# Performance work log

Hardware: AMD Instinct MI355X
Metric: run time of the kernel (lower is better)

## Reference

```python
import jax, jax.numpy as jnp
import numpy as np

B, N, M, K = 1024, 20000, 10000, 8
CHK_W, OBS_W = 8, 200          # fixed support size per check / observable row
EPS = 1e-6
BETA = 0.5


def setup_inputs() -> dict:
    rng = np.random.default_rng(0)
    # packed CSR-style support sets (fixed row weight -> dense index tables)
    chk_cols = jnp.asarray(rng.integers(0, N, size=(M, CHK_W)), dtype=jnp.int32)
    obs_cols = jnp.asarray(rng.integers(0, N, size=(K, OBS_W)), dtype=jnp.int32)
    key = jax.random.key(0)
    k1, k2, k3 = jax.random.split(key, 3)
    llrs = jax.random.normal(k1, (B, N), dtype=jnp.float32) * 2.0
    syndromes = jax.random.bernoulli(k2, 0.5, (B, M)).astype(jnp.float32)
    observables = jax.random.bernoulli(k3, 0.5, (B, K)).astype(jnp.float32)
    return {"llrs": llrs, "syndromes": syndromes, "observables": observables,
            "chk_cols": chk_cols, "obs_cols": obs_cols}


def _pred_llr(tanh_half, cols):
    # tanh_half: (B, N); cols: (R, W) -> gathered (B, R, W)
    g = tanh_half[:, cols]
    prod = jnp.prod(g, axis=-1)                       # BP check-node tanh product, (B, R)
    prod = jnp.clip(prod, -1.0 + EPS, 1.0 - EPS)
    return 2.0 * jnp.arctanh(prod)


def _bce_with_logits(z, y):
    # BCEWithLogitsLoss(z, y) = softplus(z) - z*y (numerically stable)
    return jax.nn.softplus(z) - z * y


def reference(llrs, syndromes, observables, chk_cols, obs_cols):
    t = jnp.tanh(llrs * 0.5)                          # (B, N)
    syn_pred_llr = _pred_llr(t, chk_cols)             # (B, M)
    obs_pred_llr = _pred_llr(t, obs_cols)             # (B, K)
    loss1 = _bce_with_logits(-syn_pred_llr, syndromes).sum(axis=1)
    loss2 = _bce_with_logits(-obs_pred_llr, observables).sum(axis=1)
    loss = BETA * loss1 + (1.0 - BETA) * loss2
    return loss.mean()
```

## Files before the change

### kernel.cpp

```cpp
#include <hip/hip_runtime.h>

#define B_ 1024
#define N_ 20000
#define M_ 10000
#define K_ 8
#define OBS_W_ 200
#define TPB 1024

constexpr float EPS_   = 1e-6f;
constexpr float LN2_   = 0.69314718055994530942f;
constexpr float LOG2E_ = 1.4426950408889634f;

typedef _Float16 f16x2 __attribute__((ext_vector_type(2)));
typedef _Float16 f16x8 __attribute__((ext_vector_type(8)));

__device__ __forceinline__ float tanh_half_fast(float x) {
    float e = __builtin_amdgcn_exp2f(x * LOG2E_);
    return 1.0f - 2.0f * __builtin_amdgcn_rcpf(e + 1.0f);
}

template <bool ATOMIC>
__global__ __launch_bounds__(TPB) void decode_loss_main2(
    const float* __restrict__ llrs,
    const float* __restrict__ syndromes,
    const float* __restrict__ observables,
    const int*   __restrict__ chk_cols,
    const int*   __restrict__ obs_cols,
    float* __restrict__ part)
{
    extern __shared__ char smem_raw[];
    f16x2* t2 = reinterpret_cast<f16x2*>(smem_raw);
    __shared__ float red0[TPB / 64], red1[TPB / 64];

    const int b0  = 2 * blockIdx.x;
    const int b1  = b0 + 1;
    const int tid = threadIdx.x;

    const float4* r0 = reinterpret_cast<const float4*>(llrs + (size_t)b0 * N_);
    const float4* r1 = reinterpret_cast<const float4*>(llrs + (size_t)b1 * N_);
    for (int i = tid; i < N_ / 4; i += TPB) {
        float4 a = r0[i];
        float4 c = r1[i];
        f16x8 v;
        v[0] = (_Float16)tanh_half_fast(a.x); v[1] = (_Float16)tanh_half_fast(c.x);
        v[2] = (_Float16)tanh_half_fast(a.y); v[3] = (_Float16)tanh_half_fast(c.y);
        v[4] = (_Float16)tanh_half_fast(a.z); v[5] = (_Float16)tanh_half_fast(c.z);
        v[6] = (_Float16)tanh_half_fast(a.w); v[7] = (_Float16)tanh_half_fast(c.w);
        *reinterpret_cast<f16x8*>(&t2[4 * i]) = v;
    }
    __syncthreads();

    float acc0 = 0.0f, acc1 = 0.0f;
    int   cnt  = 0;
    const float* syn0 = syndromes + (size_t)b0 * M_;
    const float* syn1 = syndromes + (size_t)b1 * M_;
    const int4*  cc   = reinterpret_cast<const int4*>(chk_cols);
    for (int m = tid; m < M_; m += TPB) {
        int4 c0 = cc[2 * m];
        int4 c1 = cc[2 * m + 1];
        f16x2 g0 = t2[c0.x], g1 = t2[c0.y], g2 = t2[c0.z], g3 = t2[c0.w];
        f16x2 g4 = t2[c1.x], g5 = t2[c1.y], g6 = t2[c1.z], g7 = t2[c1.w];
        f16x2 p  = ((g0 * g1) * (g2 * g3)) * ((g4 * g5) * (g6 * g7));
        float pa = (float)p[0];
        float pb = (float)p[1];
        pa = fminf(fmaxf(pa, -1.0f + EPS_), 1.0f - EPS_);
        pb = fminf(fmaxf(pb, -1.0f + EPS_), 1.0f - EPS_);
        float w0 = fmaf(1.0f - 2.0f * syn0[m], pa, 1.0f);
        float w1 = fmaf(1.0f - 2.0f * syn1[m], pb, 1.0f);
        acc0 += __builtin_amdgcn_logf(w0);
        acc1 += __builtin_amdgcn_logf(w1);
        ++cnt;
    }
    float sum0 = 0.5f * LN2_ * ((float)cnt - acc0);
    float sum1 = 0.5f * LN2_ * ((float)cnt - acc1);

    if (tid < 128) {
        const int row = tid >> 6;
        const int k   = (tid >> 3) & 7;
        const int seg = tid & 7;
        const int* oc = obs_cols + k * OBS_W_ + seg * 25;
        float pr = 1.0f;
        #pragma unroll 5
        for (int w = 0; w < 25; ++w) {
            f16x2 g = t2[oc[w]];
            pr *= (float)g[row];
        }
        #pragma unroll
        for (int off = 1; off < 8; off <<= 1) pr *= __shfl_xor(pr, off, 64);
        if (seg == 0) {
            const int bb = row == 0 ? b0 : b1;
            float p = fminf(fmaxf(pr, -1.0f + EPS_), 1.0f - EPS_);
            float sgn = 1.0f - 2.0f * observables[(size_t)bb * K_ + k];
            float w2  = fmaf(sgn, p, 1.0f);
            float v   = 0.5f * LN2_ * (1.0f - __builtin_amdgcn_logf(w2));
            if (row == 0) sum0 += v; else sum1 += v;
        }
    }

    for (int off = 32; off > 0; off >>= 1) {
        sum0 += __shfl_down(sum0, off, 64);
        sum1 += __shfl_down(sum1, off, 64);
    }
    const int lane = tid & 63, wv = tid >> 6;
    if (lane == 0) { red0[wv] = sum0; red1[wv] = sum1; }
    __syncthreads();
    if (tid == 0) {
        float tot = 0.0f;
        #pragma unroll
        for (int i = 0; i < TPB / 64; ++i) tot += red0[i] + red1[i];
        if (ATOMIC) {
            atomicAdd(part, tot * (1.0f / (float)B_));
        } else {
            part[blockIdx.x] = tot;
        }
    }
}

__global__ __launch_bounds__(256) void decode_loss_reduce(
    const float* __restrict__ part, float* __restrict__ out, int n)
{
    __shared__ float red[4];
    const int tid = threadIdx.x;
    float s = 0.0f;
    for (int i = tid; i < n; i += 256) s += part[i];
    for (int off = 32; off > 0; off >>= 1) s += __shfl_down(s, off, 64);
    const int lane = tid & 63, wv = tid >> 6;
    if (lane == 0) red[wv] = s;
    __syncthreads();
    if (tid == 0) out[0] = (red[0] + red[1] + red[2] + red[3]) * (1.0f / (float)B_);
}

extern "C" void kernel_launch(void* const* d_in, const int* in_sizes, int n_in,
                              void* d_out, int out_size, void* d_ws, size_t ws_size,
                              hipStream_t stream) {
    const float* llrs        = (const float*)d_in[0];
    const float* syndromes   = (const float*)d_in[1];
    const float* observables = (const float*)d_in[2];
    const int*   chk_cols    = (const int*)d_in[3];
    const int*   obs_cols    = (const int*)d_in[4];
    float*       out         = (float*)d_out;

    const size_t lds_bytes = (size_t)N_ * sizeof(f16x2);

    static_assert(sizeof(f16x2) == 4, "");
    {
        auto kf = decode_loss_main2<false>;
        auto kt = decode_loss_main2<true>;
        (void)hipFuncSetAttribute((const void*)kf,
            hipFuncAttributeMaxDynamicSharedMemorySize, (int)lds_bytes);
        (void)hipFuncSetAttribute((const void*)kt,
            hipFuncAttributeMaxDynamicSharedMemorySize, (int)lds_bytes);
    }

    const int nblk = B_ / 2;
    if (ws_size >= (size_t)nblk * sizeof(float)) {
        float* part = (float*)d_ws;
        decode_loss_main2<false><<<nblk, TPB, lds_bytes, stream>>>(
            llrs, syndromes, observables, chk_cols, obs_cols, part);
        decode_loss_reduce<<<1, 256, 0, stream>>>(part, out, nblk);
    } else {
        hipMemsetAsync(out, 0, sizeof(float), stream);
        decode_loss_main2<true><<<nblk, TPB, lds_bytes, stream>>>(
            llrs, syndromes, observables, chk_cols, obs_cols, out);
    }
}
```

Measured before the change: 29.74 us.

## Process four batch rows per block with interleaved f16x4 tanh table in LDS

Adds a kernel variant in which each block handles four batch rows instead of two. The tanh values are stored interleaved as f16x4 in 160KB of LDS, so each gather of a check column serves four samples and chk_cols is read once per four rows. The aim is to amortize index loads and LDS gather instructions over more rows. In exchange it halves the block count to 256, which may be fewer than the number of CUs, and uses more LDS per block. It falls back to the two-row kernel if the LDS attribute cannot be set.

```diff
diff --git a/kernel.cpp b/kernel.cpp
--- a/kernel.cpp
+++ b/kernel.cpp
@@ -12,11 +12,107 @@
 constexpr float LOG2E_ = 1.4426950408889634f;
 
 typedef _Float16 f16x2 __attribute__((ext_vector_type(2)));
+typedef _Float16 f16x4 __attribute__((ext_vector_type(4)));
 typedef _Float16 f16x8 __attribute__((ext_vector_type(8)));
 
 __device__ __forceinline__ float tanh_half_fast(float x) {
     float e = __builtin_amdgcn_exp2f(x * LOG2E_);
     return 1.0f - 2.0f * __builtin_amdgcn_rcpf(e + 1.0f);
+}
+
+__device__ __forceinline__ float bce_term(float p, float y) {
+    p = fminf(fmaxf(p, -1.0f + EPS_), 1.0f - EPS_);
+    float w = fmaf(1.0f - 2.0f * y, p, 1.0f);
+    return __builtin_amdgcn_logf(w);
+}
+
+template <bool ATOMIC>
+__global__ __launch_bounds__(TPB) void decode_loss_main4(
+    const float* __restrict__ llrs,
+    const float* __restrict__ syndromes,
+    const float* __restrict__ observables,
+    const int*   __restrict__ chk_cols,
+    const int*   __restrict__ obs_cols,
+    float* __restrict__ part)
+{
+    extern __shared__ char smem_raw[];
+    f16x4* t4 = reinterpret_cast<f16x4*>(smem_raw);
+    __shared__ float red[TPB / 64];
+
+    const int b0  = 4 * blockIdx.x;
+    const int tid = threadIdx.x;
+
+    const float4* r0 = reinterpret_cast<const float4*>(llrs + (size_t)(b0 + 0) * N_);
+    const float4* r1 = reinterpret_cast<const float4*>(llrs + (size_t)(b0 + 1) * N_);
+    const float4* r2 = reinterpret_cast<const float4*>(llrs + (size_t)(b0 + 2) * N_);
+    const float4* r3 = reinterpret_cast<const float4*>(llrs + (size_t)(b0 + 3) * N_);
+    for (int i = tid; i < N_ / 4; i += TPB) {
+        float4 a = r0[i], b = r1[i], c = r2[i], d = r3[i];
+        f16x8 w01, w23;
+        w01[0] = (_Float16)tanh_half_fast(a.x); w01[1] = (_Float16)tanh_half_fast(b.x);
+        w01[2] = (_Float16)tanh_half_fast(c.x); w01[3] = (_Float16)tanh_half_fast(d.x);
+        w01[4] = (_Float16)tanh_half_fast(a.y); w01[5] = (_Float16)tanh_half_fast(b.y);
+        w01[6] = (_Float16)tanh_half_fast(c.y); w01[7] = (_Float16)tanh_half_fast(d.y);
+        w23[0] = (_Float16)tanh_half_fast(a.z); w23[1] = (_Float16)tanh_half_fast(b.z);
+        w23[2] = (_Float16)tanh_half_fast(c.z); w23[3] = (_Float16)tanh_half_fast(d.z);
+        w23[4] = (_Float16)tanh_half_fast(a.w); w23[5] = (_Float16)tanh_half_fast(b.w);
+        w23[6] = (_Float16)tanh_half_fast(c.w); w23[7] = (_Float16)tanh_half_fast(d.w);
+        *reinterpret_cast<f16x8*>(&t4[4 * i + 0]) = w01;
+        *reinterpret_cast<f16x8*>(&t4[4 * i + 2]) = w23;
+    }
+    __syncthreads();
+
+    float acc = 0.0f;
+    int   cnt = 0;
+    const float* syn0 = syndromes + (size_t)(b0 + 0) * M_;
+    const float* syn1 = syndromes + (size_t)(b0 + 1) * M_;
+    const float* syn2 = syndromes + (size_t)(b0 + 2) * M_;
+    const float* syn3 = syndromes + (size_t)(b0 + 3) * M_;
+    const int4*  cc   = reinterpret_cast<const int4*>(chk_cols);
+    for (int m = tid; m < M_; m += TPB) {
+        int4 c0 = cc[2 * m];
+        int4 c1 = cc[2 * m + 1];
+        f16x4 g0 = t4[c0.x], g1 = t4[c0.y], g2 = t4[c0.z], g3 = t4[c0.w];
+        f16x4 g4 = t4[c1.x], g5 = t4[c1.y], g6 = t4[c1.z], g7 = t4[c1.w];
+        f16x4 p  = ((g0 * g1) * (g2 * g3)) * ((g4 * g5) * (g6 * g7));
+        acc += bce_term((float)p[0], syn0[m]);
+        acc += bce_term((float)p[1], syn1[m]);
+        acc += bce_term((float)p[2], syn2[m]);
+        acc += bce_term((float)p[3], syn3[m]);
+        ++cnt;
+    }
+    float sum = 0.5f * LN2_ * (4.0f * (float)cnt - acc);
+
+    if (tid < 256) {
+        const int row = tid >> 6;
+        const int k   = (tid >> 3) & 7;
+        const int seg = tid & 7;
+        const int* oc = obs_cols + k * OBS_W_ + seg * 25;
+        float pr = 1.0f;
+        #pragma unroll 5
+        for (int w = 0; w < 25; ++w) {
+            f16x4 g = t4[oc[w]];
+            pr *= (float)g[row];
+        }
+        #pragma unroll
+        for (int off = 1; off < 8; off <<= 1) pr *= __shfl_xor(pr, off, 64);
+        if (seg == 0) {
+            float y = observables[(size_t)(b0 + row) * K_ + k];
+            sum += 0.5f * LN2_ * (1.0f - bce_term(pr, y));
+        }
+    }
+
+    for (int off = 32; off > 0; off >>= 1) sum += __shfl_down(sum, off, 64);
+    const int lane = tid & 63, wv = tid >> 6;
+    if (lane == 0) red[wv] = sum;
+    __syncthreads();
+    if (tid == 0) {
+        float tot = 0.0f;
+        #pragma unroll
+        for (int i = 0; i < TPB / 64; ++i) tot += red[i];
+        if (ATOMIC) atomicAdd(part, tot * (1.0f / (float)B_));
+        else        part[blockIdx.x] = tot;
+    }
 }
 
 template <bool ATOMIC>
@@ -30,17 +126,15 @@
 {
     extern __shared__ char smem_raw[];
     f16x2* t2 = reinterpret_cast<f16x2*>(smem_raw);
-    __shared__ float red0[TPB / 64], red1[TPB / 64];
+    __shared__ float red[TPB / 64];
 
     const int b0  = 2 * blockIdx.x;
-    const int b1  = b0 + 1;
     const int tid = threadIdx.x;
 
     const float4* r0 = reinterpret_cast<const float4*>(llrs + (size_t)b0 * N_);
-    const float4* r1 = reinterpret_cast<const float4*>(llrs + (size_t)b1 * N_);
+    const float4* r1 = reinterpret_cast<const float4*>(llrs + (size_t)(b0 + 1) * N_);
     for (int i = tid; i < N_ / 4; i += TPB) {
-        float4 a = r0[i];
-        float4 c = r1[i];
+        float4 a = r0[i], c = r1[i];
         f16x8 v;
         v[0] = (_Float16)tanh_half_fast(a.x); v[1] = (_Float16)tanh_half_fast(c.x);
         v[2] = (_Float16)tanh_half_fast(a.y); v[3] = (_Float16)tanh_half_fast(c.y);
@@ -50,10 +144,10 @@
     }
     __syncthreads();
 
-    float acc0 = 0.0f, acc1 = 0.0f;
-    int   cnt  = 0;
+    float acc = 0.0f;
+    int   cnt = 0;
     const float* syn0 = syndromes + (size_t)b0 * M_;
-    const float* syn1 = syndromes + (size_t)b1 * M_;
+    const float* syn1 = syndromes + (size_t)(b0 + 1) * M_;
     const int4*  cc   = reinterpret_cast<const int4*>(chk_cols);
     for (int m = tid; m < M_; m += TPB) {
         int4 c0 = cc[2 * m];
@@ -61,18 +155,11 @@
         f16x2 g0 = t2[c0.x], g1 = t2[c0.y], g2 = t2[c0.z], g3 = t2[c0.w];
         f16x2 g4 = t2[c1.x], g5 = t2[c1.y], g6 = t2[c1.z], g7 = t2[c1.w];
         f16x2 p  = ((g0 * g1) * (g2 * g3)) * ((g4 * g5) * (g6 * g7));
-        float pa = (float)p[0];
-        float pb = (float)p[1];
-        pa = fminf(fmaxf(pa, -1.0f + EPS_), 1.0f - EPS_);
-        pb = fminf(fmaxf(pb, -1.0f + EPS_), 1.0f - EPS_);
-        float w0 = fmaf(1.0f - 2.0f * syn0[m], pa, 1.0f);
-        float w1 = fmaf(1.0f - 2.0f * syn1[m], pb, 1.0f);
-        acc0 += __builtin_amdgcn_logf(w0);
-        acc1 += __builtin_amdgcn_logf(w1);
+        acc += bce_term((float)p[0], syn0[m]);
+        acc += bce_term((float)p[1], syn1[m]);
         ++cnt;
     }
-    float sum0 = 0.5f * LN2_ * ((float)cnt - acc0);
-    float sum1 = 0.5f * LN2_ * ((float)cnt - acc1);
+    float sum = 0.5f * LN2_ * (2.0f * (float)cnt - acc);
 
     if (tid < 128) {
         const int row = tid >> 6;
@@ -81,38 +168,25 @@
         const int* oc = obs_cols + k * OBS_W_ + seg * 25;
         float pr = 1.0f;
         #pragma unroll 5
-        for (int w = 0; w < 25; ++w) {
-            f16x2 g = t2[oc[w]];
-            pr *= (float)g[row];
-        }
+        for (int w = 0; w < 25; ++w) { f16x2 g = t2[oc[w]]; pr *= (float)g[row]; }
         #pragma unroll
         for (int off = 1; off < 8; off <<= 1) pr *= __shfl_xor(pr, off, 64);
         if (seg == 0) {
-            const int bb = row == 0 ? b0 : b1;
-            float p = fminf(fmaxf(pr, -1.0f + EPS_), 1.0f - EPS_);
-            float sgn = 1.0f - 2.0f * observables[(size_t)bb * K_ + k];
-            float w2  = fmaf(sgn, p, 1.0f);
-            float v   = 0.5f * LN2_ * (1.0f - __builtin_amdgcn_logf(w2));
-            if (row == 0) sum0 += v; else sum1 += v;
+            float y = observables[(size_t)(b0 + row) * K_ + k];
+            sum += 0.5f * LN2_ * (1.0f - bce_term(pr, y));
         }
     }
 
-    for (int off = 32; off > 0; off >>= 1) {
-        sum0 += __shfl_down(sum0, off, 64);
-        sum1 += __shfl_down(sum1, off, 64);
-    }
+    for (int off = 32; off > 0; off >>= 1) sum += __shfl_down(sum, off, 64);
     const int lane = tid & 63, wv = tid >> 6;
-    if (lane == 0) { red0[wv] = sum0; red1[wv] = sum1; }
+    if (lane == 0) red[wv] = sum;
     __syncthreads();
     if (tid == 0) {
         float tot = 0.0f;
         #pragma unroll
-        for (int i = 0; i < TPB / 64; ++i) tot += red0[i] + red1[i];
-        if (ATOMIC) {
-            atomicAdd(part, tot * (1.0f / (float)B_));
-        } else {
-            part[blockIdx.x] = tot;
-        }
+        for (int i = 0; i < TPB / 64; ++i) tot += red[i];
+        if (ATOMIC) atomicAdd(part, tot * (1.0f / (float)B_));
+        else        part[blockIdx.x] = tot;
     }
 }
 
@@ -140,27 +214,39 @@
     const int*   obs_cols    = (const int*)d_in[4];
     float*       out         = (float*)d_out;
 
-    const size_t lds_bytes = (size_t)N_ * sizeof(f16x2);
-
-    static_assert(sizeof(f16x2) == 4, "");
-    {
-        auto kf = decode_loss_main2<false>;
-        auto kt = decode_loss_main2<true>;
-        (void)hipFuncSetAttribute((const void*)kf,
-            hipFuncAttributeMaxDynamicSharedMemorySize, (int)lds_bytes);
-        (void)hipFuncSetAttribute((const void*)kt,
-            hipFuncAttributeMaxDynamicSharedMemorySize, (int)lds_bytes);
-    }
-
-    const int nblk = B_ / 2;
+    const size_t lds4 = (size_t)N_ * sizeof(f16x4);
+    const size_t lds2 = (size_t)N_ * sizeof(f16x2);
+
+    hipError_t e4 = hipFuncSetAttribute((const void*)decode_loss_main4<false>,
+        hipFuncAttributeMaxDynamicSharedMemorySize, (int)lds4);
+    (void)hipFuncSetAttribute((const void*)decode_loss_main4<true>,
+        hipFuncAttributeMaxDynamicSharedMemorySize, (int)lds4);
+
+    const bool use4 = (e4 == hipSuccess);
+    if (!use4) {
+        (void)hipFuncSetAttribute((const void*)decode_loss_main2<false>,
+            hipFuncAttributeMaxDynamicSharedMemorySize, (int)lds2);
+        (void)hipFuncSetAttribute((const void*)decode_loss_main2<true>,
+            hipFuncAttributeMaxDynamicSharedMemorySize, (int)lds2);
+    }
+
+    const int nblk = use4 ? B_ / 4 : B_ / 2;
     if (ws_size >= (size_t)nblk * sizeof(float)) {
         float* part = (float*)d_ws;
-        decode_loss_main2<false><<<nblk, TPB, lds_bytes, stream>>>(
-            llrs, syndromes, observables, chk_cols, obs_cols, part);
+        if (use4)
+            decode_loss_main4<false><<<nblk, TPB, lds4, stream>>>(
+                llrs, syndromes, observables, chk_cols, obs_cols, part);
+        else
+            decode_loss_main2<false><<<nblk, TPB, lds2, stream>>>(
+                llrs, syndromes, observables, chk_cols, obs_cols, part);
         decode_loss_reduce<<<1, 256, 0, stream>>>(part, out, nblk);
     } else {
         hipMemsetAsync(out, 0, sizeof(float), stream);
-        decode_loss_main2<true><<<nblk, TPB, lds_bytes, stream>>>(
-            llrs, syndromes, observables, chk_cols, obs_cols, out);
-    }
-}
+        if (use4)
+            decode_loss_main4<true><<<nblk, TPB, lds4, stream>>>(
+                llrs, syndromes, observables, chk_cols, obs_cols, out);
+        else
+            decode_loss_main2<true><<<nblk, TPB, lds2, stream>>>(
+                llrs, syndromes, observables, chk_cols, obs_cols, out);
+    }
+}
```

Result: faster. 26.69 us (-10.3%).
